# Kernel tuning notes

Hardware: AMD Instinct MI355X
Metric: run time of the kernel (lower is better)

The kernel has to match this reference:

```python
import jax, jax.numpy as jnp
import numpy as np

N = 50000      # total nodes after flattening [1,1,N,D]
E = 600000     # random edges (plus N self-loops appended)
D = 128        # in_dim == out_dim
H = 8          # num_heads
DP = D // H    # per-head dim (each_out_dim)
SLOPE = 0.2    # DGL GATv2Conv default negative_slope


def setup_inputs() -> dict:
    key = jax.random.key(0)
    ks = jax.random.split(key, 6)
    x = jax.random.normal(ks[0], (1, 1, N, D), dtype=jnp.float32)
    s = 1.0 / np.sqrt(D).astype(np.float32)
    # GATv2Conv params: separate src/dst linear projections (share_weights=False),
    # with bias, plus a per-head attention vector.
    w_src = jax.random.uniform(ks[1], (D, H * DP), jnp.float32, -s, s)
    b_src = jnp.zeros((H * DP,), jnp.float32)
    w_dst = jax.random.uniform(ks[2], (D, H * DP), jnp.float32, -s, s)
    b_dst = jnp.zeros((H * DP,), jnp.float32)
    attn_w = jax.random.uniform(ks[3], (H, DP), jnp.float32, -s, s)
    self_loop = jnp.arange(N, dtype=jnp.int32)
    src = jnp.concatenate([jax.random.randint(ks[4], (E,), 0, N, dtype=jnp.int32), self_loop])
    dst = jnp.concatenate([jax.random.randint(ks[5], (E,), 0, N, dtype=jnp.int32), self_loop])
    return {"x": x, "w_src": w_src, "b_src": b_src, "w_dst": w_dst,
            "b_dst": b_dst, "attn_w": attn_w, "src": src, "dst": dst}


def reference(x, w_src, b_src, w_dst, b_dst, attn_w, src, dst):
    shape = x.shape
    h = x.reshape(-1, shape[3])                       # (N, D)
    n = h.shape[0]
    fs = (h @ w_src + b_src).reshape(n, H, DP)        # (N, H, Dp) source proj
    fd = (h @ w_dst + b_dst).reshape(n, H, DP)        # (N, H, Dp) dest proj
    # GATv2: e_ij = a^T LeakyReLU(W_s h_i + W_d h_j)
    e = jax.nn.leaky_relu(fs[src] + fd[dst], SLOPE)   # (E, H, Dp)
    logits = jnp.einsum('ehd,hd->eh', e, attn_w)      # (E, H)
    # segment softmax over incoming edges of each destination node
    m = jax.ops.segment_max(logits, dst, num_segments=n)
    m = jnp.where(jnp.isfinite(m), m, 0.0)
    ex = jnp.exp(logits - m[dst])                     # (E, H)
    denom = jax.ops.segment_sum(ex, dst, num_segments=n)
    alpha = ex / denom[dst]                           # (E, H)
    # weighted scatter-add aggregation of source features
    out = jax.ops.segment_sum(alpha[:, :, None] * fs[src], dst, num_segments=n)
    return out.reshape(shape)
```

## Files before the change

kernel.cpp:

```cpp
#include <hip/hip_runtime.h>
#include <hip/hip_bf16.h>

#define HH 8
#define DP 16
#define DD 128
#define SLOPE 0.2f

#define BM 32
__global__ __launch_bounds__(256) void proj_kernel(
    const float* __restrict__ x,
    const float* __restrict__ w_src, const float* __restrict__ b_src,
    const float* __restrict__ w_dst, const float* __restrict__ b_dst,
    float* __restrict__ fs, float* __restrict__ fd, int n) {
  __shared__ float xs[BM][DD];
  const int tid = threadIdx.x;
  const int block0 = blockIdx.x * BM;

  for (int i = tid; i < BM * DD / 4; i += 256) {
    int m = i >> 5;
    int k = (i & 31) << 2;
    int node = block0 + m;
    float4 v = make_float4(0.f, 0.f, 0.f, 0.f);
    if (node < n) v = *reinterpret_cast<const float4*>(x + (size_t)node * DD + k);
    *reinterpret_cast<float4*>(&xs[m][k]) = v;
  }
  __syncthreads();

  const int c = tid & (DD - 1);
  const int half = tid >> 7;
  const int m0 = half * 16;

  float acc_s[16], acc_d[16];
#pragma unroll
  for (int m = 0; m < 16; ++m) { acc_s[m] = 0.f; acc_d[m] = 0.f; }

  for (int k = 0; k < DD; k += 4) {
    float ws0 = w_src[(k + 0) * DD + c];
    float ws1 = w_src[(k + 1) * DD + c];
    float ws2 = w_src[(k + 2) * DD + c];
    float ws3 = w_src[(k + 3) * DD + c];
    float wd0 = w_dst[(k + 0) * DD + c];
    float wd1 = w_dst[(k + 1) * DD + c];
    float wd2 = w_dst[(k + 2) * DD + c];
    float wd3 = w_dst[(k + 3) * DD + c];
#pragma unroll
    for (int m = 0; m < 16; ++m) {
      float4 xv = *reinterpret_cast<const float4*>(&xs[m0 + m][k]);
      acc_s[m] = fmaf(xv.x, ws0, acc_s[m]);
      acc_s[m] = fmaf(xv.y, ws1, acc_s[m]);
      acc_s[m] = fmaf(xv.z, ws2, acc_s[m]);
      acc_s[m] = fmaf(xv.w, ws3, acc_s[m]);
      acc_d[m] = fmaf(xv.x, wd0, acc_d[m]);
      acc_d[m] = fmaf(xv.y, wd1, acc_d[m]);
      acc_d[m] = fmaf(xv.z, wd2, acc_d[m]);
      acc_d[m] = fmaf(xv.w, wd3, acc_d[m]);
    }
  }

  const float bs = b_src[c];
  const float bd = b_dst[c];
#pragma unroll
  for (int m = 0; m < 16; ++m) {
    int node = block0 + m0 + m;
    if (node < n) {
      fs[(size_t)node * DD + c] = acc_s[m] + bs;
      fd[(size_t)node * DD + c] = acc_d[m] + bd;
    }
  }
}

__global__ __launch_bounds__(256) void count_kernel(const int* __restrict__ dst,
                                                    int* __restrict__ count, int ecount) {
  int e = blockIdx.x * 256 + threadIdx.x;
  if (e < ecount) atomicAdd(&count[dst[e]], 1);
}

__global__ __launch_bounds__(256) void alloc_kernel(const int* __restrict__ count,
                                                    int* __restrict__ cursor,
                                                    int* __restrict__ total, int n) {
  const int lane = threadIdx.x & 63;
  const int wid = threadIdx.x >> 6;
  const int wave = blockIdx.x * 4 + wid;
  const int i0 = wave * 256;

  int excl[4];
  int carry = 0;
#pragma unroll
  for (int j = 0; j < 4; ++j) {
    int i = i0 + j * 64 + lane;
    int v = (i < n) ? count[i] : 0;
    int incl = v;
#pragma unroll
    for (int off = 1; off < 64; off <<= 1) {
      int t = __shfl_up(incl, (unsigned)off, 64);
      if (lane >= off) incl += t;
    }
    excl[j] = carry + incl - v;
    carry += __shfl(incl, 63, 64);
  }
  int base = 0;
  if (lane == 63) base = atomicAdd(total, carry);
  base = __shfl(base, 63, 64);
#pragma unroll
  for (int j = 0; j < 4; ++j) {
    int i = i0 + j * 64 + lane;
    if (i < n) cursor[i] = base + excl[j];
  }
}

__global__ __launch_bounds__(256) void scatter_kernel(const int* __restrict__ src,
                                                      const int* __restrict__ dst,
                                                      int* __restrict__ cursor,
                                                      int* __restrict__ edge_src, int ecount) {
  int e = blockIdx.x * 256 + threadIdx.x;
  if (e < ecount) {
    int pos = atomicAdd(&cursor[dst[e]], 1);
    edge_src[pos] = src[e];
  }
}

__global__ __launch_bounds__(256) void node_kernel(const float* __restrict__ fs,
                                                   const float* __restrict__ fd,
                                                   const float* __restrict__ attn_w,
                                                   const int* __restrict__ cursor,
                                                   const int* __restrict__ count,
                                                   const int* __restrict__ edge_src,
                                                   float* __restrict__ out, int n) {
  const int wid = threadIdx.x >> 6;
  const int lane = threadIdx.x & 63;
  const int node = blockIdx.x * 4 + wid;
  if (node >= n) return;

  const int d0 = lane * 2;
  const float2 aw = *reinterpret_cast<const float2*>(&attn_w[d0]);
  const float2 fdv = *reinterpret_cast<const float2*>(&fd[(size_t)node * DD + d0]);

  const int e1 = cursor[node];
  const int e0 = e1 - count[node];

  float m0 = -1e30f, m1 = -1e30f;
  float den0 = 0.f, den1 = 0.f;
  float2 ac0 = make_float2(0.f, 0.f), ac1 = make_float2(0.f, 0.f);

  int e = e0;
  for (; e + 1 < e1; e += 2) {
    int sA = edge_src[e];
    int sB = edge_src[e + 1];
    float2 fA = *reinterpret_cast<const float2*>(&fs[(size_t)sA * DD + d0]);
    float2 fB = *reinterpret_cast<const float2*>(&fs[(size_t)sB * DD + d0]);

    float a0 = fA.x + fdv.x; a0 = (a0 > 0.f) ? a0 : a0 * SLOPE;
    float a1 = fA.y + fdv.y; a1 = (a1 > 0.f) ? a1 : a1 * SLOPE;
    float b0 = fB.x + fdv.x; b0 = (b0 > 0.f) ? b0 : b0 * SLOPE;
    float b1 = fB.y + fdv.y; b1 = (b1 > 0.f) ? b1 : b1 * SLOPE;
    float pA = aw.x * a0 + aw.y * a1;
    float pB = aw.x * b0 + aw.y * b1;
    pA += __shfl_xor(pA, 1, 64); pB += __shfl_xor(pB, 1, 64);
    pA += __shfl_xor(pA, 2, 64); pB += __shfl_xor(pB, 2, 64);
    pA += __shfl_xor(pA, 4, 64); pB += __shfl_xor(pB, 4, 64);

    float mA = fmaxf(m0, pA);
    float scA = __expf(m0 - mA);
    float eA = __expf(pA - mA);
    den0 = den0 * scA + eA;
    ac0.x = ac0.x * scA + eA * fA.x;
    ac0.y = ac0.y * scA + eA * fA.y;
    m0 = mA;

    float mB = fmaxf(m1, pB);
    float scB = __expf(m1 - mB);
    float eB = __expf(pB - mB);
    den1 = den1 * scB + eB;
    ac1.x = ac1.x * scB + eB * fB.x;
    ac1.y = ac1.y * scB + eB * fB.y;
    m1 = mB;
  }
  if (e < e1) {
    int sA = edge_src[e];
    float2 fA = *reinterpret_cast<const float2*>(&fs[(size_t)sA * DD + d0]);
    float a0 = fA.x + fdv.x; a0 = (a0 > 0.f) ? a0 : a0 * SLOPE;
    float a1 = fA.y + fdv.y; a1 = (a1 > 0.f) ? a1 : a1 * SLOPE;
    float pA = aw.x * a0 + aw.y * a1;
    pA += __shfl_xor(pA, 1, 64);
    pA += __shfl_xor(pA, 2, 64);
    pA += __shfl_xor(pA, 4, 64);
    float mA = fmaxf(m0, pA);
    float scA = __expf(m0 - mA);
    float eA = __expf(pA - mA);
    den0 = den0 * scA + eA;
    ac0.x = ac0.x * scA + eA * fA.x;
    ac0.y = ac0.y * scA + eA * fA.y;
    m0 = mA;
  }

  float M = fmaxf(m0, m1);
  float s0 = __expf(m0 - M);
  float s1 = __expf(m1 - M);
  float denom = den0 * s0 + den1 * s1;
  float ax = ac0.x * s0 + ac1.x * s1;
  float ay = ac0.y * s0 + ac1.y * s1;

  float inv = (denom > 0.f) ? 1.f / denom : 0.f;
  *reinterpret_cast<float2*>(&out[(size_t)node * DD + d0]) =
      make_float2(ax * inv, ay * inv);
}

extern "C" void kernel_launch(void* const* d_in, const int* in_sizes, int n_in,
                              void* d_out, int out_size, void* d_ws, size_t ws_size,
                              hipStream_t stream) {
  const float* x      = (const float*)d_in[0];
  const float* w_src  = (const float*)d_in[1];
  const float* b_src  = (const float*)d_in[2];
  const float* w_dst  = (const float*)d_in[3];
  const float* b_dst  = (const float*)d_in[4];
  const float* attn_w = (const float*)d_in[5];
  const int* src = (const int*)d_in[6];
  const int* dst = (const int*)d_in[7];
  float* out = (float*)d_out;

  const int n = in_sizes[0] / DD;
  const int ecount = in_sizes[6];

  size_t off = 0;
  float* fs = (float*)((char*)d_ws + off); off += (size_t)n * DD * sizeof(float);
  float* fd = (float*)((char*)d_ws + off); off += (size_t)n * DD * sizeof(float);
  int* edge_src = (int*)((char*)d_ws + off); off += (size_t)ecount * sizeof(int);
  int* cursor   = (int*)((char*)d_ws + off); off += (size_t)n * sizeof(int);
  int* count    = (int*)((char*)d_ws + off); off += (size_t)n * sizeof(int);
  int* total    = (int*)((char*)d_ws + off); off += sizeof(int);
  (void)ws_size;

  hipMemsetAsync(count, 0, (size_t)(n + 1) * sizeof(int), stream);

  proj_kernel<<<(n + BM - 1) / BM, 256, 0, stream>>>(x, w_src, b_src, w_dst, b_dst, fs, fd, n);
  count_kernel<<<(ecount + 255) / 256, 256, 0, stream>>>(dst, count, ecount);
  alloc_kernel<<<(n + 1023) / 1024, 256, 0, stream>>>(count, cursor, total, n);
  scatter_kernel<<<(ecount + 255) / 256, 256, 0, stream>>>(src, dst, cursor, edge_src, ecount);
  node_kernel<<<(n + 3) / 4, 256, 0, stream>>>(fs, fd, attn_w, cursor, count, edge_src, out, n);
}
```

Baseline: 270.6 us.

## Fuse degree counting into projection kernel, prefetch weights, unroll node loop by four

Merges the edge-degree count into the projection launch by giving the first 512 blocks the atomic counting work, which removes one kernel launch and lets counting overlap with the GEMM. The projection loop now loads the next four weight rows while computing on the current ones, a software prefetch that hides global load latency. The node aggregation loop handles four edges per iteration with four independent online-softmax accumulators, exposing more memory-level parallelism for the gathered rows at the cost of extra registers.

```diff
diff --git a/kernel.cpp b/kernel.cpp
--- a/kernel.cpp
+++ b/kernel.cpp
@@ -7,14 +7,24 @@
 #define SLOPE 0.2f
 
 #define BM 32
-__global__ __launch_bounds__(256) void proj_kernel(
+#define COUNT_BLOCKS 512
+__global__ __launch_bounds__(256) void proj_count_kernel(
     const float* __restrict__ x,
     const float* __restrict__ w_src, const float* __restrict__ b_src,
     const float* __restrict__ w_dst, const float* __restrict__ b_dst,
-    float* __restrict__ fs, float* __restrict__ fd, int n) {
+    float* __restrict__ fs, float* __restrict__ fd, int n,
+    const int* __restrict__ dst, int* __restrict__ count, int ecount) {
   __shared__ float xs[BM][DD];
   const int tid = threadIdx.x;
-  const int block0 = blockIdx.x * BM;
+
+  if (blockIdx.x < COUNT_BLOCKS) {
+    const int stride = COUNT_BLOCKS * 256;
+    for (int e = blockIdx.x * 256 + tid; e < ecount; e += stride)
+      atomicAdd(&count[dst[e]], 1);
+    return;
+  }
+
+  const int block0 = (blockIdx.x - COUNT_BLOCKS) * BM;
 
   for (int i = tid; i < BM * DD / 4; i += 256) {
     int m = i >> 5;
@@ -27,22 +37,23 @@
   __syncthreads();
 
   const int c = tid & (DD - 1);
-  const int half = tid >> 7;
-  const int m0 = half * 16;
+  const int m0 = (tid >> 7) * 16;
 
   float acc_s[16], acc_d[16];
 #pragma unroll
   for (int m = 0; m < 16; ++m) { acc_s[m] = 0.f; acc_d[m] = 0.f; }
 
+  float ws0 = w_src[0 * DD + c], ws1 = w_src[1 * DD + c];
+  float ws2 = w_src[2 * DD + c], ws3 = w_src[3 * DD + c];
+  float wd0 = w_dst[0 * DD + c], wd1 = w_dst[1 * DD + c];
+  float wd2 = w_dst[2 * DD + c], wd3 = w_dst[3 * DD + c];
+
   for (int k = 0; k < DD; k += 4) {
-    float ws0 = w_src[(k + 0) * DD + c];
-    float ws1 = w_src[(k + 1) * DD + c];
-    float ws2 = w_src[(k + 2) * DD + c];
-    float ws3 = w_src[(k + 3) * DD + c];
-    float wd0 = w_dst[(k + 0) * DD + c];
-    float wd1 = w_dst[(k + 1) * DD + c];
-    float wd2 = w_dst[(k + 2) * DD + c];
-    float wd3 = w_dst[(k + 3) * DD + c];
+    const int kn = (k + 4) & (DD - 1);
+    float nws0 = w_src[(kn + 0) * DD + c], nws1 = w_src[(kn + 1) * DD + c];
+    float nws2 = w_src[(kn + 2) * DD + c], nws3 = w_src[(kn + 3) * DD + c];
+    float nwd0 = w_dst[(kn + 0) * DD + c], nwd1 = w_dst[(kn + 1) * DD + c];
+    float nwd2 = w_dst[(kn + 2) * DD + c], nwd3 = w_dst[(kn + 3) * DD + c];
 #pragma unroll
     for (int m = 0; m < 16; ++m) {
       float4 xv = *reinterpret_cast<const float4*>(&xs[m0 + m][k]);
@@ -55,6 +66,8 @@
       acc_d[m] = fmaf(xv.z, wd2, acc_d[m]);
       acc_d[m] = fmaf(xv.w, wd3, acc_d[m]);
     }
+    ws0 = nws0; ws1 = nws1; ws2 = nws2; ws3 = nws3;
+    wd0 = nwd0; wd1 = nwd1; wd2 = nwd2; wd3 = nwd3;
   }
 
   const float bs = b_src[c];
@@ -67,12 +80,6 @@
       fd[(size_t)node * DD + c] = acc_d[m] + bd;
     }
   }
-}
-
-__global__ __launch_bounds__(256) void count_kernel(const int* __restrict__ dst,
-                                                    int* __restrict__ count, int ecount) {
-  int e = blockIdx.x * 256 + threadIdx.x;
-  if (e < ecount) atomicAdd(&count[dst[e]], 1);
 }
 
 __global__ __launch_bounds__(256) void alloc_kernel(const int* __restrict__ count,
@@ -138,67 +145,60 @@
   const int e1 = cursor[node];
   const int e0 = e1 - count[node];
 
-  float m0 = -1e30f, m1 = -1e30f;
-  float den0 = 0.f, den1 = 0.f;
-  float2 ac0 = make_float2(0.f, 0.f), ac1 = make_float2(0.f, 0.f);
+  float mx[4] = {-1e30f, -1e30f, -1e30f, -1e30f};
+  float den[4] = {0.f, 0.f, 0.f, 0.f};
+  float2 ac[4] = {{0.f, 0.f}, {0.f, 0.f}, {0.f, 0.f}, {0.f, 0.f}};
+
+  auto logit_of = [&](float2 fsv) -> float {
+    float t0 = fsv.x + fdv.x; t0 = (t0 > 0.f) ? t0 : t0 * SLOPE;
+    float t1 = fsv.y + fdv.y; t1 = (t1 > 0.f) ? t1 : t1 * SLOPE;
+    float p = aw.x * t0 + aw.y * t1;
+    p += __shfl_xor(p, 1, 64);
+    p += __shfl_xor(p, 2, 64);
+    p += __shfl_xor(p, 4, 64);
+    return p;
+  };
+  auto upd = [](float& m, float& dn, float2& a, float logit, float2 fsv) {
+    float mn = fmaxf(m, logit);
+    float sc = __expf(m - mn);
+    float p = __expf(logit - mn);
+    dn = dn * sc + p;
+    a.x = a.x * sc + p * fsv.x;
+    a.y = a.y * sc + p * fsv.y;
+    m = mn;
+  };
 
   int e = e0;
-  for (; e + 1 < e1; e += 2) {
-    int sA = edge_src[e];
-    int sB = edge_src[e + 1];
-    float2 fA = *reinterpret_cast<const float2*>(&fs[(size_t)sA * DD + d0]);
-    float2 fB = *reinterpret_cast<const float2*>(&fs[(size_t)sB * DD + d0]);
-
-    float a0 = fA.x + fdv.x; a0 = (a0 > 0.f) ? a0 : a0 * SLOPE;
-    float a1 = fA.y + fdv.y; a1 = (a1 > 0.f) ? a1 : a1 * SLOPE;
-    float b0 = fB.x + fdv.x; b0 = (b0 > 0.f) ? b0 : b0 * SLOPE;
-    float b1 = fB.y + fdv.y; b1 = (b1 > 0.f) ? b1 : b1 * SLOPE;
-    float pA = aw.x * a0 + aw.y * a1;
-    float pB = aw.x * b0 + aw.y * b1;
-    pA += __shfl_xor(pA, 1, 64); pB += __shfl_xor(pB, 1, 64);
-    pA += __shfl_xor(pA, 2, 64); pB += __shfl_xor(pB, 2, 64);
-    pA += __shfl_xor(pA, 4, 64); pB += __shfl_xor(pB, 4, 64);
-
-    float mA = fmaxf(m0, pA);
-    float scA = __expf(m0 - mA);
-    float eA = __expf(pA - mA);
-    den0 = den0 * scA + eA;
-    ac0.x = ac0.x * scA + eA * fA.x;
-    ac0.y = ac0.y * scA + eA * fA.y;
-    m0 = mA;
-
-    float mB = fmaxf(m1, pB);
-    float scB = __expf(m1 - mB);
-    float eB = __expf(pB - mB);
-    den1 = den1 * scB + eB;
-    ac1.x = ac1.x * scB + eB * fB.x;
-    ac1.y = ac1.y * scB + eB * fB.y;
-    m1 = mB;
-  }
-  if (e < e1) {
-    int sA = edge_src[e];
-    float2 fA = *reinterpret_cast<const float2*>(&fs[(size_t)sA * DD + d0]);
-    float a0 = fA.x + fdv.x; a0 = (a0 > 0.f) ? a0 : a0 * SLOPE;
-    float a1 = fA.y + fdv.y; a1 = (a1 > 0.f) ? a1 : a1 * SLOPE;
-    float pA = aw.x * a0 + aw.y * a1;
-    pA += __shfl_xor(pA, 1, 64);
-    pA += __shfl_xor(pA, 2, 64);
-    pA += __shfl_xor(pA, 4, 64);
-    float mA = fmaxf(m0, pA);
-    float scA = __expf(m0 - mA);
-    float eA = __expf(pA - mA);
-    den0 = den0 * scA + eA;
-    ac0.x = ac0.x * scA + eA * fA.x;
-    ac0.y = ac0.y * scA + eA * fA.y;
-    m0 = mA;
-  }
-
-  float M = fmaxf(m0, m1);
-  float s0 = __expf(m0 - M);
-  float s1 = __expf(m1 - M);
-  float denom = den0 * s0 + den1 * s1;
-  float ax = ac0.x * s0 + ac1.x * s1;
-  float ay = ac0.y * s0 + ac1.y * s1;
+  for (; e + 3 < e1; e += 4) {
+    int s0 = edge_src[e], s1 = edge_src[e + 1];
+    int s2 = edge_src[e + 2], s3 = edge_src[e + 3];
+    float2 f0 = *reinterpret_cast<const float2*>(&fs[(size_t)s0 * DD + d0]);
+    float2 f1 = *reinterpret_cast<const float2*>(&fs[(size_t)s1 * DD + d0]);
+    float2 f2 = *reinterpret_cast<const float2*>(&fs[(size_t)s2 * DD + d0]);
+    float2 f3 = *reinterpret_cast<const float2*>(&fs[(size_t)s3 * DD + d0]);
+    float l0 = logit_of(f0), l1 = logit_of(f1);
+    float l2 = logit_of(f2), l3 = logit_of(f3);
+    upd(mx[0], den[0], ac[0], l0, f0);
+    upd(mx[1], den[1], ac[1], l1, f1);
+    upd(mx[2], den[2], ac[2], l2, f2);
+    upd(mx[3], den[3], ac[3], l3, f3);
+  }
+  for (; e < e1; ++e) {
+    int s0 = edge_src[e];
+    float2 f0 = *reinterpret_cast<const float2*>(&fs[(size_t)s0 * DD + d0]);
+    float l0 = logit_of(f0);
+    upd(mx[0], den[0], ac[0], l0, f0);
+  }
+
+  float M = fmaxf(fmaxf(mx[0], mx[1]), fmaxf(mx[2], mx[3]));
+  float denom = 0.f, ax = 0.f, ay = 0.f;
+#pragma unroll
+  for (int j = 0; j < 4; ++j) {
+    float s = __expf(mx[j] - M);
+    denom += den[j] * s;
+    ax += ac[j].x * s;
+    ay += ac[j].y * s;
+  }
 
   float inv = (denom > 0.f) ? 1.f / denom : 0.f;
   *reinterpret_cast<float2*>(&out[(size_t)node * DD + d0]) =
@@ -232,8 +232,9 @@
 
   hipMemsetAsync(count, 0, (size_t)(n + 1) * sizeof(int), stream);
 
-  proj_kernel<<<(n + BM - 1) / BM, 256, 0, stream>>>(x, w_src, b_src, w_dst, b_dst, fs, fd, n);
-  count_kernel<<<(ecount + 255) / 256, 256, 0, stream>>>(dst, count, ecount);
+  const int proj_blocks = (n + BM - 1) / BM;
+  proj_count_kernel<<<COUNT_BLOCKS + proj_blocks, 256, 0, stream>>>(
+      x, w_src, b_src, w_dst, b_dst, fs, fd, n, dst, count, ecount);
   alloc_kernel<<<(n + 1023) / 1024, 256, 0, stream>>>(count, cursor, total, n);
   scatter_kernel<<<(ecount + 255) / 256, 256, 0, stream>>>(src, dst, cursor, edge_src, ecount);
   node_kernel<<<(n + 3) / 4, 256, 0, stream>>>(fs, fd, attn_w, cursor, count, edge_src, out, n);
```

New measurement: 264.2 us. 2.4% less time.
